# Kernel optimization log

Measured on AMD Instinct MI355X. Metric: run time of the kernel, lower is better.

Reference implementation:

```python
import jax, jax.numpy as jnp
import numpy as np

VOCAB = 10000
N_NODES = 50000
D = 256
N_TYPES = 3
N_LAYERS = 4
E_PER_TYPE = 300000


def setup_inputs() -> dict:
    key = jax.random.key(0)
    k1, k2, k3, k4 = jax.random.split(key, 4)
    node_label_ids = jax.random.randint(k1, (N_NODES,), 0, VOCAB)
    adjacency_lists = jax.random.randint(k2, (N_TYPES, E_PER_TYPE, 2), 0, N_NODES)
    emb_table = jax.random.normal(k3, (VOCAB, D), dtype=jnp.float32)
    # scale ~ glorot so 4 relu layers don't blow up
    layer_weights = jax.random.normal(k4, (N_LAYERS, N_TYPES, D, D), dtype=jnp.float32) / jnp.sqrt(jnp.float32(D))
    return {
        "node_label_ids": node_label_ids,
        "adjacency_lists": adjacency_lists,
        "emb_table": emb_table,
        "layer_weights": layer_weights,
    }


def reference(node_label_ids, adjacency_lists, emb_table, layer_weights):
    n_nodes = node_label_ids.shape[0]
    # embedding lookup (node label -> initial node state); emb dim == hidden dim
    h = emb_table[node_label_ids]  # [N, D]
    n_layers, n_types = layer_weights.shape[0], layer_weights.shape[1]
    for l in range(n_layers):
        agg = jnp.zeros_like(h)
        for t in range(n_types):
            src = adjacency_lists[t, :, 0]
            tgt = adjacency_lists[t, :, 1]
            # gather source states, per-edge-type linear message transform
            msg = h[src] @ layer_weights[l, t]  # [E, D]
            # scatter-sum messages onto target nodes
            agg = agg + jax.ops.segment_sum(msg, tgt, num_segments=n_nodes)
        h = jax.nn.relu(agg)
    return h
```

## Files before the change

kernel.cpp:

```cpp
#include <hip/hip_runtime.h>

#define NN 50000
#define DD 256
#define NT 3
#define NL 4
#define EPT 300000
#define KK 768
#define SCAN_BLOCKS 196
#define MROWS 50048

typedef __attribute__((ext_vector_type(8))) short bf16x8;
typedef __attribute__((ext_vector_type(4))) float f32x4;
typedef __attribute__((ext_vector_type(4))) unsigned int u32x4;

__device__ __forceinline__ unsigned short f2bf(float f) {
  unsigned u = __builtin_bit_cast(unsigned, f);
  unsigned r = u + 0x7fffu + ((u >> 16) & 1u);
  return (unsigned short)(r >> 16);
}
__device__ __forceinline__ float bflo2f(unsigned u) {
  return __builtin_bit_cast(float, u << 16);
}
__device__ __forceinline__ float bfhi2f(unsigned u) {
  return __builtin_bit_cast(float, u & 0xffff0000u);
}

__global__ void gather_emb(const int* __restrict__ labels,
                           const float* __restrict__ emb,
                           unsigned short* __restrict__ h) {
  int node = blockIdx.x;
  int lane = threadIdx.x;
  float4 v = ((const float4*)(emb + (size_t)labels[node] * DD))[lane];
  unsigned a = (unsigned)f2bf(v.x) | ((unsigned)f2bf(v.y) << 16);
  unsigned b = (unsigned)f2bf(v.z) | ((unsigned)f2bf(v.w) << 16);
  ((uint2*)(h + (size_t)node * DD))[lane] = make_uint2(a, b);
}

__global__ void zero_kernel(float* __restrict__ p, int n4) {
  int i = blockIdx.x * blockDim.x + threadIdx.x;
  int stride = gridDim.x * blockDim.x;
  float4* p4 = (float4*)p;
  for (; i < n4; i += stride) p4[i] = make_float4(0.f, 0.f, 0.f, 0.f);
}

__global__ __launch_bounds__(256) void wconv(const float* __restrict__ Wl,
                                             unsigned short* __restrict__ WT) {
  int i = blockIdx.x * 256 + threadIdx.x;
  int l = i / (DD * KK);
  int rem = i % (DD * KK);
  int n = rem / KK;
  int kk = rem % KK;
  int t = kk >> 8;
  int k = kk & 255;
  float v = Wl[((size_t)(l * NT + t) * DD + k) * DD + n];
  WT[i] = f2bf(v);
}

__global__ __launch_bounds__(256) void hist_kernel(const int* __restrict__ adj,
                                                   int* __restrict__ counts) {
  int t = blockIdx.y;
  int e = blockIdx.x * 256 + threadIdx.x;
  if (e >= EPT) return;
  int tgt = adj[(size_t)t * EPT * 2 + 2 * e + 1];
  atomicAdd(&counts[t * NN + tgt], 1);
}

__global__ __launch_bounds__(256) void scan1(const int* __restrict__ counts,
                                             int* __restrict__ rowptr,
                                             int* __restrict__ bsums) {
  int t = blockIdx.y, b = blockIdx.x;
  int i = b * 256 + threadIdx.x;
  int v = (i < NN) ? counts[t * NN + i] : 0;
  __shared__ int s[256];
  s[threadIdx.x] = v;
  __syncthreads();
  for (int off = 1; off < 256; off <<= 1) {
    int y = (threadIdx.x >= off) ? s[threadIdx.x - off] : 0;
    __syncthreads();
    s[threadIdx.x] += y;
    __syncthreads();
  }
  if (i < NN) rowptr[t * (NN + 1) + i] = s[threadIdx.x] - v;
  if (threadIdx.x == 255) bsums[t * SCAN_BLOCKS + b] = s[255];
}

__global__ __launch_bounds__(256) void scan2(int* __restrict__ bsums) {
  int t = blockIdx.x;
  int v = (threadIdx.x < SCAN_BLOCKS) ? bsums[t * SCAN_BLOCKS + threadIdx.x] : 0;
  __shared__ int s[256];
  s[threadIdx.x] = v;
  __syncthreads();
  for (int off = 1; off < 256; off <<= 1) {
    int y = (threadIdx.x >= off) ? s[threadIdx.x - off] : 0;
    __syncthreads();
    s[threadIdx.x] += y;
    __syncthreads();
  }
  if (threadIdx.x < SCAN_BLOCKS) bsums[t * SCAN_BLOCKS + threadIdx.x] = s[threadIdx.x] - v;
}

__global__ __launch_bounds__(256) void scan3(int* __restrict__ rowptr,
                                             const int* __restrict__ bsums,
                                             int* __restrict__ cursor) {
  int t = blockIdx.y, b = blockIdx.x;
  int i = b * 256 + threadIdx.x;
  if (i < NN) {
    int r = rowptr[t * (NN + 1) + i] + bsums[t * SCAN_BLOCKS + b];
    rowptr[t * (NN + 1) + i] = r;
    cursor[t * NN + i] = r;
  }
  if (b == 0 && threadIdx.x == 0) rowptr[t * (NN + 1) + NN] = EPT;
}

__global__ __launch_bounds__(256) void bucket_kernel(const int* __restrict__ adj,
                                                     int* __restrict__ cursor,
                                                     int* __restrict__ esrc) {
  int t = blockIdx.y;
  int e = blockIdx.x * 256 + threadIdx.x;
  if (e >= EPT) return;
  int s = adj[(size_t)t * EPT * 2 + 2 * e];
  int tgt = adj[(size_t)t * EPT * 2 + 2 * e + 1];
  int pos = atomicAdd(&cursor[t * NN + tgt], 1);
  esrc[(size_t)t * EPT + pos] = s;
}

__global__ __launch_bounds__(256) void agg_csr(const int* __restrict__ rowptr,
                                               const int* __restrict__ esrc,
                                               const unsigned short* __restrict__ h,
                                               unsigned short* __restrict__ Gcat) {
  int t = blockIdx.y;
  int node = blockIdx.x * 8 + (threadIdx.x >> 5);
  if (node >= NN) return;
  int sub = threadIdx.x & 31;
  const int* rp = rowptr + t * (NN + 1);
  const int* es = esrc + (size_t)t * EPT;
  int e = rp[node];
  int end = rp[node + 1];
  const u32x4* h4 = (const u32x4*)h;
  float a0 = 0.f, a1 = 0.f, a2 = 0.f, a3 = 0.f, a4 = 0.f, a5 = 0.f, a6 = 0.f, a7 = 0.f;
  for (; e + 3 < end; e += 4) {
    u32x4 v0 = h4[(size_t)es[e] * 32 + sub];
    u32x4 v1 = h4[(size_t)es[e + 1] * 32 + sub];
    u32x4 v2 = h4[(size_t)es[e + 2] * 32 + sub];
    u32x4 v3 = h4[(size_t)es[e + 3] * 32 + sub];
    a0 += (bflo2f(v0.x) + bflo2f(v1.x)) + (bflo2f(v2.x) + bflo2f(v3.x));
    a1 += (bfhi2f(v0.x) + bfhi2f(v1.x)) + (bfhi2f(v2.x) + bfhi2f(v3.x));
    a2 += (bflo2f(v0.y) + bflo2f(v1.y)) + (bflo2f(v2.y) + bflo2f(v3.y));
    a3 += (bfhi2f(v0.y) + bfhi2f(v1.y)) + (bfhi2f(v2.y) + bfhi2f(v3.y));
    a4 += (bflo2f(v0.z) + bflo2f(v1.z)) + (bflo2f(v2.z) + bflo2f(v3.z));
    a5 += (bfhi2f(v0.z) + bfhi2f(v1.z)) + (bfhi2f(v2.z) + bfhi2f(v3.z));
    a6 += (bflo2f(v0.w) + bflo2f(v1.w)) + (bflo2f(v2.w) + bflo2f(v3.w));
    a7 += (bfhi2f(v0.w) + bfhi2f(v1.w)) + (bfhi2f(v2.w) + bfhi2f(v3.w));
  }
  for (; e < end; ++e) {
    u32x4 v0 = h4[(size_t)es[e] * 32 + sub];
    a0 += bflo2f(v0.x);
    a1 += bfhi2f(v0.x);
    a2 += bflo2f(v0.y);
    a3 += bfhi2f(v0.y);
    a4 += bflo2f(v0.z);
    a5 += bfhi2f(v0.z);
    a6 += bflo2f(v0.w);
    a7 += bfhi2f(v0.w);
  }
  u32x4 o;
  o.x = (unsigned)f2bf(a0) | ((unsigned)f2bf(a1) << 16);
  o.y = (unsigned)f2bf(a2) | ((unsigned)f2bf(a3) << 16);
  o.z = (unsigned)f2bf(a4) | ((unsigned)f2bf(a5) << 16);
  o.w = (unsigned)f2bf(a6) | ((unsigned)f2bf(a7) << 16);
  ((u32x4*)(Gcat + (size_t)node * KK + t * DD))[sub] = o;
}

template <int OUTF32>
__global__ __launch_bounds__(512, 4) void gemm_bf16(const unsigned short* __restrict__ A,
                                                    const unsigned short* __restrict__ BT,
                                                    void* __restrict__ Cout) {
  __shared__ __align__(16) char lds[49152];
  const int tid = threadIdx.x;
  const int w = tid >> 6, lane = tid & 63;
  const int m0 = blockIdx.x * 128;
  const int wm = (w >> 2) * 64, wn = (w & 3) * 64;
  const int r15 = lane & 15;
  const int g16 = (lane >> 4) * 16;

  f32x4 acc[4][4] = {};
  const char* Ab = (const char*)A;
  const char* Bb = (const char*)BT;

  const int arow = tid >> 2;
  const int acol = (tid & 3) * 32;
  const int asw = (arow & 7) << 4;
  const int brow = tid >> 1;
  const int bcol = (tid & 1) * 64;
  const int bsw = (brow & 7) << 4;
  u32x4 ra[2], rb[4];

  const int NTK = KK / 64;

#define GLOAD(kt)                                                            \
  {                                                                          \
    const char* ap = Ab + (size_t)(m0 + arow) * (KK * 2) + (size_t)(kt)*128; \
    const char* bp = Bb + (size_t)brow * (KK * 2) + (size_t)(kt)*128;        \
    ra[0] = *(const u32x4*)(ap + acol);                                      \
    ra[1] = *(const u32x4*)(ap + acol + 16);                                 \
    _Pragma("unroll") for (int p = 0; p < 4; p++) rb[p] =                    \
        *(const u32x4*)(bp + bcol + p * 16);                                 \
  }
#define SWRITE()                                                             \
  {                                                                          \
    *(u32x4*)(lds + arow * 128 + (acol ^ asw)) = ra[0];                      \
    *(u32x4*)(lds + arow * 128 + ((acol + 16) ^ asw)) = ra[1];               \
    _Pragma("unroll") for (int p = 0; p < 4; p++) *(u32x4*)(                 \
        lds + 16384 + brow * 128 + ((bcol + p * 16) ^ bsw)) = rb[p];         \
  }

  GLOAD(0);
  SWRITE();
  __syncthreads();
  for (int kt = 0; kt < NTK; ++kt) {
    if (kt + 1 < NTK) GLOAD(kt + 1);
#pragma unroll
    for (int ks = 0; ks < 2; ++ks) {
      bf16x8 af[4], bfr[4];
#pragma unroll
      for (int mf = 0; mf < 4; ++mf) {
        int row = wm + mf * 16 + r15;
        af[mf] = *(const bf16x8*)(lds + row * 128 + ((ks * 64 + g16) ^ ((row & 7) << 4)));
      }
#pragma unroll
      for (int nf = 0; nf < 4; ++nf) {
        int row = wn + nf * 16 + r15;
        bfr[nf] =
            *(const bf16x8*)(lds + 16384 + row * 128 + ((ks * 64 + g16) ^ ((row & 7) << 4)));
      }
#pragma unroll
      for (int mf = 0; mf < 4; ++mf)
#pragma unroll
        for (int nf = 0; nf < 4; ++nf)
          acc[mf][nf] =
              __builtin_amdgcn_mfma_f32_16x16x32_bf16(af[mf], bfr[nf], acc[mf][nf], 0, 0, 0);
    }
    if (kt + 1 < NTK) {
      __syncthreads();
      SWRITE();
      __syncthreads();
    }
  }

#pragma unroll
  for (int mf = 0; mf < 4; ++mf) {
#pragma unroll
    for (int r = 0; r < 4; ++r) {
      int grow = m0 + wm + mf * 16 + (lane >> 4) * 4 + r;
      if (grow >= NN) continue;
#pragma unroll
      for (int nf = 0; nf < 4; ++nf) {
        int gcol = wn + nf * 16 + r15;
        float v = fmaxf(acc[mf][nf][r], 0.f);
        if (OUTF32)
          ((float*)Cout)[(size_t)grow * DD + gcol] = v;
        else
          ((unsigned short*)Cout)[(size_t)grow * DD + gcol] = f2bf(v);
      }
    }
  }
#undef GLOAD
#undef SWRITE
}

extern "C" void kernel_launch(void* const* d_in, const int* in_sizes, int n_in,
                              void* d_out, int out_size, void* d_ws, size_t ws_size,
                              hipStream_t stream) {
  const int* labels = (const int*)d_in[0];
  const int* adj = (const int*)d_in[1];
  const float* emb = (const float*)d_in[2];
  const float* Wl = (const float*)d_in[3];

  char* base = (char*)d_ws;
  unsigned short* h = (unsigned short*)base;
  size_t off = (size_t)NN * DD * 2;
  unsigned short* Gcat = (unsigned short*)(base + off);
  off += (size_t)MROWS * KK * 2;
  unsigned short* WT = (unsigned short*)(base + off);
  off += (size_t)NL * DD * KK * 2;
  int* rowptr = (int*)(base + off);
  off += (size_t)((NT * (NN + 1) * 4 + 15) & ~15);
  int* esrc = (int*)(base + off);

  int* counts = (int*)Gcat;
  int* cursor = (int*)((char*)Gcat + (1 << 20));
  int* bsums = (int*)((char*)Gcat + (2 << 20));

  wconv<<<(NL * DD * KK) / 256, 256, 0, stream>>>(Wl, WT);
  gather_emb<<<NN, 64, 0, stream>>>(labels, emb, h);

  zero_kernel<<<256, 256, 0, stream>>>((float*)counts, (3 * NN) / 4);
  {
    dim3 g((EPT + 255) / 256, NT);
    hist_kernel<<<g, 256, 0, stream>>>(adj, counts);
  }
  {
    dim3 g(SCAN_BLOCKS, NT);
    scan1<<<g, 256, 0, stream>>>(counts, rowptr, bsums);
  }
  scan2<<<NT, 256, 0, stream>>>(bsums);
  {
    dim3 g(SCAN_BLOCKS, NT);
    scan3<<<g, 256, 0, stream>>>(rowptr, bsums, cursor);
  }
  {
    dim3 g((EPT + 255) / 256, NT);
    bucket_kernel<<<g, 256, 0, stream>>>(adj, cursor, esrc);
  }

  dim3 ga((NN + 7) / 8, NT);
  const int gg = MROWS / 128;
  for (int l = 0; l < NL; ++l) {
    agg_csr<<<ga, 256, 0, stream>>>(rowptr, esrc, h, Gcat);
    const unsigned short* WTl = WT + (size_t)l * DD * KK;
    if (l < NL - 1)
      gemm_bf16<0><<<gg, 512, 0, stream>>>(Gcat, WTl, h);
    else
      gemm_bf16<1><<<gg, 512, 0, stream>>>(Gcat, WTl, d_out);
  }
}
```

Baseline: 517.7 us.

## Load GEMM tiles directly to LDS with pre-swizzled global layouts

The gather kernel and the weight conversion now write A and B already XOR-swizzled in global memory. This lets the GEMM copy tiles straight from global memory into LDS with global_load_lds, skipping the staging through registers. The aim is to save VGPRs and the LDS write instructions. In exchange, the next tile's load no longer overlaps with the MFMA work: it is issued between two barriers, so load latency is exposed on every k-step.

```diff
diff --git a/kernel.cpp b/kernel.cpp
--- a/kernel.cpp
+++ b/kernel.cpp
@@ -53,7 +53,7 @@
   int t = kk >> 8;
   int k = kk & 255;
   float v = Wl[((size_t)(l * NT + t) * DD + k) * DD + n];
-  WT[i] = f2bf(v);
+  WT[(size_t)l * DD * KK + (size_t)n * KK + (kk ^ ((n & 7) << 3))] = f2bf(v);
 }
 
 __global__ __launch_bounds__(256) void hist_kernel(const int* __restrict__ adj,
@@ -168,8 +168,13 @@
   o.y = (unsigned)f2bf(a2) | ((unsigned)f2bf(a3) << 16);
   o.z = (unsigned)f2bf(a4) | ((unsigned)f2bf(a5) << 16);
   o.w = (unsigned)f2bf(a6) | ((unsigned)f2bf(a7) << 16);
-  ((u32x4*)(Gcat + (size_t)node * KK + t * DD))[sub] = o;
-}
+  ((u32x4*)(Gcat + (size_t)node * KK + t * DD))[sub ^ (node & 7)] = o;
+}
+
+#define GLL(g, l)                                                     \
+  __builtin_amdgcn_global_load_lds(                                   \
+      (const __attribute__((address_space(1))) unsigned int*)(g),     \
+      (__attribute__((address_space(3))) unsigned int*)(l), 16, 0, 0)
 
 template <int OUTF32>
 __global__ __launch_bounds__(512, 4) void gemm_bf16(const unsigned short* __restrict__ A,
@@ -187,38 +192,28 @@
   const char* Ab = (const char*)A;
   const char* Bb = (const char*)BT;
 
-  const int arow = tid >> 2;
-  const int acol = (tid & 3) * 32;
-  const int asw = (arow & 7) << 4;
-  const int brow = tid >> 1;
-  const int bcol = (tid & 1) * 64;
-  const int bsw = (brow & 7) << 4;
-  u32x4 ra[2], rb[4];
+  const int lrow = lane >> 3;
+  const int lcol = (lane & 7) * 16;
 
   const int NTK = KK / 64;
 
-#define GLOAD(kt)                                                            \
-  {                                                                          \
-    const char* ap = Ab + (size_t)(m0 + arow) * (KK * 2) + (size_t)(kt)*128; \
-    const char* bp = Bb + (size_t)brow * (KK * 2) + (size_t)(kt)*128;        \
-    ra[0] = *(const u32x4*)(ap + acol);                                      \
-    ra[1] = *(const u32x4*)(ap + acol + 16);                                 \
-    _Pragma("unroll") for (int p = 0; p < 4; p++) rb[p] =                    \
-        *(const u32x4*)(bp + bcol + p * 16);                                 \
-  }
-#define SWRITE()                                                             \
-  {                                                                          \
-    *(u32x4*)(lds + arow * 128 + (acol ^ asw)) = ra[0];                      \
-    *(u32x4*)(lds + arow * 128 + ((acol + 16) ^ asw)) = ra[1];               \
-    _Pragma("unroll") for (int p = 0; p < 4; p++) *(u32x4*)(                 \
-        lds + 16384 + brow * 128 + ((bcol + p * 16) ^ bsw)) = rb[p];         \
-  }
-
-  GLOAD(0);
-  SWRITE();
+#define LOADTILE(kt)                                                                   \
+  {                                                                                    \
+    _Pragma("unroll") for (int i = 0; i < 2; ++i) {                                    \
+      const char* g =                                                                  \
+          Ab + (size_t)(m0 + w * 16 + i * 8 + lrow) * (KK * 2) + (size_t)(kt)*128 + lcol; \
+      GLL(g, lds + (w * 16 + i * 8) * 128);                                            \
+    }                                                                                  \
+    _Pragma("unroll") for (int j = 0; j < 4; ++j) {                                    \
+      const char* g =                                                                  \
+          Bb + (size_t)(w * 32 + j * 8 + lrow) * (KK * 2) + (size_t)(kt)*128 + lcol;   \
+      GLL(g, lds + 16384 + (w * 32 + j * 8) * 128);                                    \
+    }                                                                                  \
+  }
+
+  LOADTILE(0);
   __syncthreads();
   for (int kt = 0; kt < NTK; ++kt) {
-    if (kt + 1 < NTK) GLOAD(kt + 1);
 #pragma unroll
     for (int ks = 0; ks < 2; ++ks) {
       bf16x8 af[4], bfr[4];
@@ -242,7 +237,7 @@
     }
     if (kt + 1 < NTK) {
       __syncthreads();
-      SWRITE();
+      LOADTILE(kt + 1);
       __syncthreads();
     }
   }
@@ -264,8 +259,7 @@
       }
     }
   }
-#undef GLOAD
-#undef SWRITE
+#undef LOADTILE
 }
 
 extern "C" void kernel_launch(void* const* d_in, const int* in_sizes, int n_in,
```

Result: faster. 502.1 us (-3.0%).
